# Optimization experiments

Measured on AMD Instinct MI355X. Metric: run time of the kernel, lower is better.

The kernel has to match this reference:

```python
import jax, jax.numpy as jnp
import numpy as np

N_NODES = 50000
N_EDGES = 600000
D_IN = 128
D_HID = 128
N_IDX = 4096


def gcn_conv(x, W, b, edge_index, num_nodes):
    """PyG GCNConv: add self loops, symmetric deg normalization, scatter-add, bias."""
    h = x @ W  # [N, D_out]
    loop = jnp.arange(num_nodes, dtype=edge_index.dtype)
    src = jnp.concatenate([edge_index[0], loop])
    dst = jnp.concatenate([edge_index[1], loop])
    deg = jax.ops.segment_sum(jnp.ones_like(dst, dtype=h.dtype), dst, num_segments=num_nodes)
    dinv = jnp.where(deg > 0, jax.lax.rsqrt(jnp.maximum(deg, 1.0)), 0.0)
    norm = dinv[src] * dinv[dst]  # [E+N]
    msgs = h[src] * norm[:, None]
    out = jax.ops.segment_sum(msgs, dst, num_segments=num_nodes)
    return out + b


def setup_inputs() -> dict:
    key = jax.random.key(0)
    ks = jax.random.split(key, 18)
    d = {
        "x": jax.random.normal(ks[0], (N_NODES, D_IN), dtype=jnp.float32),
        "syntactic_edge_index": jax.random.randint(ks[1], (2, N_EDGES), 0, N_NODES, dtype=jnp.int32),
        "sequential_edge_index": jax.random.randint(ks[2], (2, N_EDGES), 0, N_NODES, dtype=jnp.int32),
        "semantic_edge_index": jax.random.randint(ks[3], (2, N_EDGES), 0, N_NODES, dtype=jnp.int32),
        "index": jax.random.randint(ks[4], (N_IDX,), 0, N_NODES, dtype=jnp.int32),
    }
    s = 1.0 / np.sqrt(D_IN)
    names = ["syn", "seq", "sem"]
    for i, n in enumerate(names):
        d[f"w1_{n}"] = jax.random.uniform(ks[5 + i], (D_IN, D_HID), jnp.float32, -s, s)
        d[f"b1_{n}"] = jnp.zeros((D_HID,), jnp.float32)
        d[f"w2_{n}"] = jax.random.uniform(ks[8 + i], (D_HID, D_HID), jnp.float32, -s, s)
        d[f"b2_{n}"] = jnp.zeros((D_HID,), jnp.float32)
    return d


def reference(x, syntactic_edge_index, sequential_edge_index, semantic_edge_index, index,
              w1_syn, b1_syn, w1_seq, b1_seq, w1_sem, b1_sem,
              w2_syn, b2_syn, w2_seq, b2_seq, w2_sem, b2_sem):
    n = x.shape[0]
    # layer 1: three parallel GCN branches + ReLU (dropout is identity in eval mode)
    a = jax.nn.relu(gcn_conv(x, w1_syn, b1_syn, syntactic_edge_index, n))
    b = jax.nn.relu(gcn_conv(x, w1_seq, b1_seq, sequential_edge_index, n))
    c = jax.nn.relu(gcn_conv(x, w1_sem, b1_sem, semantic_edge_index, n))
    h = jnp.maximum(jnp.maximum(a, b), c)
    # layer 2
    a2 = jax.nn.relu(gcn_conv(h, w2_syn, b2_syn, syntactic_edge_index, n))
    b2 = jax.nn.relu(gcn_conv(h, w2_seq, b2_seq, sequential_edge_index, n))
    c2 = jax.nn.relu(gcn_conv(h, w2_sem, b2_sem, semantic_edge_index, n))
    out = jnp.maximum(jnp.maximum(a2, b2), c2)
    return out[index]
```

## Files before the change

kernel.cpp:

```cpp
#include <hip/hip_runtime.h>
#include <hip/hip_fp16.h>

#define NN 50000
#define NE 600000
#define NG 3
#define D  128
#define NI 4096
#define BW 1024
#define NBUCK 49
#define EPT_BIN 16
#define EPB_BIN (256 * EPT_BIN)
#define NBLK_BIN ((NE + EPB_BIN - 1) / EPB_BIN)
#define XCVT_BLKS 3125
#define WCVT_BLKS 48
#define CNT_BLKS (NBLK_BIN * NG)

typedef _Float16 half8 __attribute__((ext_vector_type(8)));
typedef _Float16 half4v __attribute__((ext_vector_type(4)));
typedef float floatx4 __attribute__((ext_vector_type(4)));

static __device__ __forceinline__ float wextract(unsigned int v) {
  unsigned short u = (unsigned short)(v >> 16);
  _Float16 h;
  __builtin_memcpy(&h, &u, 2);
  return (float)h;
}

static __device__ __forceinline__ unsigned int packsw(int s, float w) {
  _Float16 h = (_Float16)w;
  unsigned short u;
  __builtin_memcpy(&u, &h, 2);
  return (unsigned int)s | ((unsigned int)u << 16);
}

static __device__ __forceinline__ int bucket_scan(const int* bcnt, int g, int lane) {
  int v = (lane < NBUCK) ? bcnt[g * NBUCK + lane] : 0;
  int incl = v;
#pragma unroll
  for (int off = 1; off < 64; off <<= 1) {
    int t = __shfl_up(incl, off, 64);
    if (lane >= off) incl += t;
  }
  return incl - v;
}


__global__ __launch_bounds__(256) void prep_kernel(
    const float* __restrict__ x, __half* __restrict__ xh,
    const float* __restrict__ W0, const float* __restrict__ W1, const float* __restrict__ W2,
    const float* __restrict__ W3, const float* __restrict__ W4, const float* __restrict__ W5,
    __half* __restrict__ Wf,
    const int* __restrict__ e0, const int* __restrict__ e1, const int* __restrict__ e2,
    int* __restrict__ bucketCnt) {
  __shared__ int cnt[NBUCK];
  int blk = blockIdx.x;
  int tid = threadIdx.x;
  if (blk < XCVT_BLKS) {
    int i = blk * 256 + tid;
    size_t base = (size_t)i * 8;
    float4 v0 = *(const float4*)&x[base];
    float4 v1 = *(const float4*)&x[base + 4];
    half8 h;
    h[0] = (_Float16)v0.x; h[1] = (_Float16)v0.y; h[2] = (_Float16)v0.z; h[3] = (_Float16)v0.w;
    h[4] = (_Float16)v1.x; h[5] = (_Float16)v1.y; h[6] = (_Float16)v1.z; h[7] = (_Float16)v1.w;
    *(half8*)&xh[base] = h;
  } else if (blk < XCVT_BLKS + WCVT_BLKS) {
    const float* Wm[6] = {W0, W1, W2, W3, W4, W5};
    int t = (blk - XCVT_BLKS) * 256 + tid;
    int mat = t >> 11;
    int fr = (t >> 6) & 31;
    int lane = t & 63;
    int tt = fr >> 2, ks = fr & 3;
    int n = tt * 16 + (lane & 15);
    int kb = ks * 32 + (lane >> 4) * 8;
    const float* W = Wm[mat];
#pragma unroll
    for (int j = 0; j < 8; j++)
      Wf[(size_t)t * 8 + j] = __float2half(W[(kb + j) * 128 + n]);
  } else {
    int cb = blk - XCVT_BLKS - WCVT_BLKS;
    int g = cb / NBLK_BIN, eb = cb % NBLK_BIN;
    const int* ei = (g == 0) ? e0 : ((g == 1) ? e1 : e2);
    if (tid < NBUCK) cnt[tid] = 0;
    __syncthreads();
    int base = eb * EPB_BIN;
#pragma unroll
    for (int i = 0; i < EPT_BIN; i++) {
      int e = base + tid + i * 256;
      if (e < NE) atomicAdd(&cnt[ei[NE + e] >> 10], 1);
    }
    __syncthreads();
    if (tid < NBUCK) atomicAdd(&bucketCnt[g * NBUCK + tid], cnt[tid]);
  }
}

__global__ __launch_bounds__(256) void bin_kernel(const int* __restrict__ e0,
    const int* __restrict__ e1, const int* __restrict__ e2,
    const int* __restrict__ bcnt, int* __restrict__ cur0,
    unsigned int* __restrict__ binned) {
  __shared__ int cnt[4][NBUCK];
  __shared__ int sbase[NBUCK];
  __shared__ int base[NBUCK];
  __shared__ int woff[4][NBUCK];
  int g = blockIdx.y;
  const int* ei = (g == 0) ? e0 : ((g == 1) ? e1 : e2);
  int tid = threadIdx.x;
  int wave = tid >> 6;
  if (tid < 64) {
    int ex = bucket_scan(bcnt, g, tid);
    if (tid < NBUCK) sbase[tid] = ex;
  }
  if (tid < NBUCK) { cnt[0][tid] = 0; cnt[1][tid] = 0; cnt[2][tid] = 0; cnt[3][tid] = 0; }
  __syncthreads();
  int estart = blockIdx.x * EPB_BIN;
  int src[EPT_BIN], dst[EPT_BIN], rk[EPT_BIN];
#pragma unroll
  for (int i = 0; i < EPT_BIN; i++) {
    int e = estart + tid + i * 256;
    if (e < NE) {
      src[i] = ei[e];
      dst[i] = ei[NE + e];
      rk[i] = atomicAdd(&cnt[wave][dst[i] >> 10], 1);
    } else {
      rk[i] = -1;
    }
  }
  __syncthreads();
  if (tid < NBUCK) {
    int c0 = cnt[0][tid], c1 = cnt[1][tid], c2 = cnt[2][tid], c3 = cnt[3][tid];
    int total = c0 + c1 + c2 + c3;
    int wb = (total > 0) ? atomicAdd(&cur0[g * NBUCK + tid], total) : 0;
    base[tid] = sbase[tid] + wb;
    woff[0][tid] = 0; woff[1][tid] = c0; woff[2][tid] = c0 + c1; woff[3][tid] = c0 + c1 + c2;
  }
  __syncthreads();
#pragma unroll
  for (int i = 0; i < EPT_BIN; i++) {
    if (rk[i] >= 0) {
      int b = dst[i] >> 10;
      binned[(size_t)g * NE + base[b] + woff[wave][b] + rk[i]] =
          (unsigned int)src[i] | ((unsigned int)dst[i] << 16);
    }
  }
}

__global__ __launch_bounds__(256) void csr_kernel(const unsigned int* __restrict__ binned,
    const int* __restrict__ bcnt, int* __restrict__ rp, float* __restrict__ dinv) {
  __shared__ int deg[BW];
  __shared__ int wsum[4];
  __shared__ int sbb;
  int g = blockIdx.y, b = blockIdx.x;
  int tid = threadIdx.x;
  int node0 = b * BW;
  if (tid < 64) {
    int ex = bucket_scan(bcnt, g, tid);
    if (tid == b) sbb = ex;
  }
  if (b == 0 && tid == 0) rp[g * (NN + 1) + NN] = NE;
  for (int i = tid; i < BW; i += 256) deg[i] = 0;
  __syncthreads();
  int bb = sbb;
  int total = bcnt[g * NBUCK + b];
  const unsigned int* bp = binned + (size_t)g * NE + bb;
  for (int e = tid; e < total; e += 256) {
    unsigned int p = bp[e];
    atomicAdd(&deg[(int)(p >> 16) - node0], 1);
  }
  __syncthreads();
  int d0 = deg[tid * 4], d1 = deg[tid * 4 + 1], d2 = deg[tid * 4 + 2], d3 = deg[tid * 4 + 3];
  int s = d0 + d1 + d2 + d3;
  int lane = tid & 63;
  int incl = s;
#pragma unroll
  for (int off = 1; off < 64; off <<= 1) {
    int n = __shfl_up(incl, off, 64);
    if (lane >= off) incl += n;
  }
  if (lane == 63) wsum[tid >> 6] = incl;
  __syncthreads();
  int wbase = 0;
#pragma unroll
  for (int w = 0; w < 4; w++)
    if (w < (tid >> 6)) wbase += wsum[w];
  int ex = wbase + incl - s;
  int exs[4] = {ex, ex + d0, ex + d0 + d1, ex + d0 + d1 + d2};
  int ds[4] = {d0, d1, d2, d3};
#pragma unroll
  for (int k = 0; k < 4; k++) {
    int node = node0 + tid * 4 + k;
    if (node < NN) {
      rp[g * (NN + 1) + node] = bb + exs[k];
      dinv[g * NN + node] = rsqrtf((float)ds[k] + 1.0f);
    }
  }
}

__global__ __launch_bounds__(256) void fillp_kernel(const unsigned int* __restrict__ binned,
    const int* __restrict__ bcnt, const int* __restrict__ rp,
    const float* __restrict__ dinv, unsigned int* __restrict__ colp) {
  __shared__ int cur[BW];
  __shared__ int sbb;
  int g = blockIdx.y, b = blockIdx.x;
  int tid = threadIdx.x;
  int node0 = b * BW;
  if (tid < 64) {
    int ex = bucket_scan(bcnt, g, tid);
    if (tid == b) sbb = ex;
  }
  for (int i = tid; i < BW; i += 256) {
    int node = node0 + i;
    cur[i] = (node < NN) ? rp[g * (NN + 1) + node] : 0;
  }
  __syncthreads();
  int bb = sbb;
  int total = bcnt[g * NBUCK + b];
  const unsigned int* bp = binned + (size_t)g * NE + bb;
  for (int e = tid; e < total; e += 256) {
    unsigned int p = bp[e];
    int srcid = (int)(p & 0xffffu);
    int r = atomicAdd(&cur[(int)(p >> 16) - node0], 1);
    colp[(size_t)g * NE + r] = packsw(srcid, dinv[g * NN + srcid]);
  }
}


__global__ __launch_bounds__(256) void aggb_kernel(
    const __half* __restrict__ srch, const int* __restrict__ rp,
    const unsigned int* __restrict__ colp, const float* __restrict__ dinv,
    const int* __restrict__ index, __half* __restrict__ tout, int nrows) {
  int b = blockIdx.y;
  int w = (blockIdx.x * 256 + threadIdx.x) >> 6;
  if (w >= nrows) return;
  int lane = threadIdx.x & 63;
  int sub = lane >> 5;
  int fl = lane & 31;
  int node = index ? index[w] : w;
  const _Float16* srcv = (const _Float16*)srch;
  half4v selfh = *(const half4v*)&srcv[(size_t)node * D + fl * 4];
  float di = dinv[b * NN + node];
  float a[4];
#pragma unroll
  for (int k = 0; k < 4; k++) a[k] = sub ? 0.f : di * (float)selfh[k];
  const int* rpb = rp + b * (NN + 1);
  int s = rpb[node], e = rpb[node + 1];
  int n = e - s;
  const unsigned int* cp = colp + (size_t)b * NE;
  unsigned int c = (lane < n) ? cp[s + lane] : 0u;
  int m = min(n, 64);
  for (int j = 0; j < m; j += 16) {
    unsigned int v[8];
    float wg[8];
    half4v h[8];
#pragma unroll
    for (int u = 0; u < 8; u++) {
      v[u] = (unsigned int)__shfl((int)c, j + u * 2 + sub, 64);
      wg[u] = wextract(v[u]);
      h[u] = *(const half4v*)&srcv[(size_t)(v[u] & 0xffffu) * D + fl * 4];
    }
#pragma unroll
    for (int u = 0; u < 8; u++)
#pragma unroll
      for (int k = 0; k < 4; k++) a[k] = fmaf((float)h[u][k], wg[u], a[k]);
  }
  for (int q = s + 64; q < e; q += 64) {
    int nn = min(e - q, 64);
    unsigned int cc = (lane < nn) ? cp[q + lane] : 0u;
    for (int j = 0; j < nn; j += 2) {
      unsigned int v = (unsigned int)__shfl((int)cc, j + sub, 64);
      float wf = wextract(v);
      half4v hv = *(const half4v*)&srcv[(size_t)(v & 0xffffu) * D + fl * 4];
#pragma unroll
      for (int k = 0; k < 4; k++) a[k] = fmaf((float)hv[k], wf, a[k]);
    }
  }
#pragma unroll
  for (int k = 0; k < 4; k++) a[k] += __shfl_xor(a[k], 32, 64);
  if (sub == 0) {
    half4v o;
#pragma unroll
    for (int k = 0; k < 4; k++) o[k] = (_Float16)(di * a[k]);
    _Float16* tv = (_Float16*)tout;
    *(half4v*)&tv[(size_t)b * nrows * D + (size_t)w * D + fl * 4] = o;
  }
}


#define ALD 136

__global__ __launch_bounds__(256) void mmf_kernel(const __half* __restrict__ A,
    const __half* __restrict__ Wf,
    const float* __restrict__ B0, const float* __restrict__ B1, const float* __restrict__ B2,
    __half* __restrict__ outh, float* __restrict__ outf, int M) {
  __shared__ _Float16 As[128 * ALD];
  __shared__ _Float16 Ws[16384];
  const float* Bb[3] = {B0, B1, B2};
  const int tid = threadIdx.x;
  const int wave = tid >> 6, lane = tid & 63;
  const int wr = (wave >> 1) * 64, wc = (wave & 1) * 64;
  const int ln = lane & 15, quad = lane >> 4;
  const int row0 = blockIdx.x * 128;
  float om[4][4][4];

  for (int b = 0; b < 3; b++) {
    const __half* Wb = Wf + (size_t)b * 16384;
#pragma unroll
    for (int i = 0; i < 8; i++) {
      int id = tid + i * 256;
      *(half8*)&Ws[id * 8] = *(const half8*)&Wb[(size_t)id * 8];
    }
    const __half* Ab = A + (size_t)b * M * D;
#pragma unroll
    for (int i = 0; i < 8; i++) {
      int idx = tid + i * 256;
      int r = idx >> 4, c8 = idx & 15;
      int gr = row0 + r;
      gr = (gr < M) ? gr : (M - 1);
      half8 v = *(const half8*)&Ab[(size_t)gr * D + c8 * 8];
      *(half8*)&As[r * ALD + c8 * 8] = v;
    }
    __syncthreads();

    float bias[4];
#pragma unroll
    for (int ct = 0; ct < 4; ct++) bias[ct] = Bb[b][wc + ct * 16 + ln];
    floatx4 acc[4][4];
#pragma unroll
    for (int rt = 0; rt < 4; rt++)
#pragma unroll
      for (int ct = 0; ct < 4; ct++)
        acc[rt][ct] = (floatx4){bias[ct], bias[ct], bias[ct], bias[ct]};

#pragma unroll
    for (int ks = 0; ks < 4; ks++) {
      half8 av[4];
#pragma unroll
      for (int rt = 0; rt < 4; rt++)
        av[rt] = *(const half8*)&As[(wr + rt * 16 + ln) * ALD + ks * 32 + quad * 8];
#pragma unroll
      for (int ct = 0; ct < 4; ct++) {
        int tt = (wc >> 4) + ct;
        half8 bv = *(const half8*)&Ws[((tt * 4 + ks) * 64 + lane) * 8];
#pragma unroll
        for (int rt = 0; rt < 4; rt++)
          acc[rt][ct] = __builtin_amdgcn_mfma_f32_16x16x32_f16(av[rt], bv, acc[rt][ct], 0, 0, 0);
      }
    }
#pragma unroll
    for (int rt = 0; rt < 4; rt++)
#pragma unroll
      for (int ct = 0; ct < 4; ct++)
#pragma unroll
        for (int r = 0; r < 4; r++) {
          float v = fmaxf(acc[rt][ct][r], 0.f);
          om[rt][ct][r] = (b == 0) ? v : fmaxf(om[rt][ct][r], v);
        }
    __syncthreads();
  }
#pragma unroll
  for (int rt = 0; rt < 4; rt++) {
    int m = row0 + wr + rt * 16 + quad * 4;
#pragma unroll
    for (int r = 0; r < 4; r++) {
      if (m + r < M) {
#pragma unroll
        for (int ct = 0; ct < 4; ct++) {
          int n = wc + ct * 16 + ln;
          if (outh) outh[(size_t)(m + r) * D + n] = __float2half(om[rt][ct][r]);
          else      outf[(size_t)(m + r) * D + n] = om[rt][ct][r];
        }
      }
    }
  }
}


extern "C" void kernel_launch(void* const* d_in, const int* in_sizes, int n_in,
                              void* d_out, int out_size, void* d_ws, size_t ws_size,
                              hipStream_t stream) {
  const float* x = (const float*)d_in[0];
  const int* e0 = (const int*)d_in[1];
  const int* e1 = (const int*)d_in[2];
  const int* e2 = (const int*)d_in[3];
  const int* index = (const int*)d_in[4];
  const float* w1[3] = {(const float*)d_in[5], (const float*)d_in[9],  (const float*)d_in[13]};
  const float* b1[3] = {(const float*)d_in[6], (const float*)d_in[10], (const float*)d_in[14]};
  const float* w2[3] = {(const float*)d_in[7], (const float*)d_in[11], (const float*)d_in[15]};
  const float* b2[3] = {(const float*)d_in[8], (const float*)d_in[12], (const float*)d_in[16]};
  float* out = (float*)d_out;

  char* ws = (char*)d_ws;
  size_t o = 0;
  auto alloc = [&](size_t bytes) {
    o = (o + 255) & ~(size_t)255;
    void* p = ws + o;
    o += bytes;
    return p;
  };
  int*    rp     = (int*)alloc((size_t)NG * (NN + 1) * 4);
  unsigned int* colp = (unsigned int*)alloc((size_t)NG * NE * 4);
  float*  dinv   = (float*)alloc((size_t)NG * NN * 4);
  int*    bcnt   = (int*)alloc((size_t)2 * NG * NBUCK * 4);
  int*    cur0   = bcnt + NG * NBUCK;
  __half* xh     = (__half*)alloc((size_t)NN * D * 2);
  __half* Wf     = (__half*)alloc((size_t)6 * 128 * 128 * 2);
  __half* t1     = (__half*)alloc((size_t)NG * NN * D * 2);
  __half* hacc   = (__half*)alloc((size_t)NN * D * 2);
  unsigned int* binned = (unsigned int*)t1;
  __half* t2     = t1;
  (void)ws_size; (void)in_sizes; (void)n_in; (void)out_size;

  hipMemsetAsync(bcnt, 0, (size_t)2 * NG * NBUCK * 4, stream);
  prep_kernel<<<XCVT_BLKS + WCVT_BLKS + CNT_BLKS, 256, 0, stream>>>(
      x, xh, w1[0], w1[1], w1[2], w2[0], w2[1], w2[2], Wf, e0, e1, e2, bcnt);
  bin_kernel<<<dim3(NBLK_BIN, NG), 256, 0, stream>>>(e0, e1, e2, bcnt, cur0, binned);
  csr_kernel<<<dim3(NBUCK, NG), 256, 0, stream>>>(binned, bcnt, rp, dinv);
  fillp_kernel<<<dim3(NBUCK, NG), 256, 0, stream>>>(binned, bcnt, rp, dinv, colp);

  aggb_kernel<<<dim3((NN * 64 + 255) / 256, NG), 256, 0, stream>>>(
      xh, rp, colp, dinv, nullptr, t1, NN);
  mmf_kernel<<<(NN + 127) / 128, 256, 0, stream>>>(t1, Wf, b1[0], b1[1], b1[2],
                                                   hacc, nullptr, NN);
  aggb_kernel<<<dim3((NI * 64 + 255) / 256, NG), 256, 0, stream>>>(
      hacc, rp, colp, dinv, index, t2, NI);
  mmf_kernel<<<(NI + 127) / 128, 256, 0, stream>>>(t2, Wf + (size_t)3 * 16384,
                                                   b2[0], b2[1], b2[2], nullptr, out, NI);
}
```

Measured before the change: 279.1 us.

## Stage binned edges in LDS, shrink aggregation unroll, template GEMM row tile

The bin kernel now writes each block's edges into a shared-memory staging buffer ordered by bucket, then copies each bucket out contiguously. This aims to replace scattered global writes with coalesced ones. The aggregation kernel's first-chunk gather loop drops from 8 to 4 unrolled neighbours, cutting register pressure at the cost of fewer loads in flight. The GEMM kernel is templated on row tiles, and the small second-layer GEMM (4096 rows) uses 64-row blocks so more blocks are launched.

```diff
diff --git a/kernel.cpp b/kernel.cpp
--- a/kernel.cpp
+++ b/kernel.cpp
@@ -100,8 +100,11 @@
     unsigned int* __restrict__ binned) {
   __shared__ int cnt[4][NBUCK];
   __shared__ int sbase[NBUCK];
-  __shared__ int base[NBUCK];
+  __shared__ int gbase[NBUCK];
   __shared__ int woff[4][NBUCK];
+  __shared__ int tot[NBUCK];
+  __shared__ int lbase[NBUCK];
+  __shared__ unsigned int stage[EPB_BIN];
   int g = blockIdx.y;
   const int* ei = (g == 0) ? e0 : ((g == 1) ? e1 : e2);
   int tid = threadIdx.x;
@@ -129,18 +132,39 @@
   if (tid < NBUCK) {
     int c0 = cnt[0][tid], c1 = cnt[1][tid], c2 = cnt[2][tid], c3 = cnt[3][tid];
     int total = c0 + c1 + c2 + c3;
+    tot[tid] = total;
     int wb = (total > 0) ? atomicAdd(&cur0[g * NBUCK + tid], total) : 0;
-    base[tid] = sbase[tid] + wb;
+    gbase[tid] = sbase[tid] + wb;
     woff[0][tid] = 0; woff[1][tid] = c0; woff[2][tid] = c0 + c1; woff[3][tid] = c0 + c1 + c2;
+  }
+  __syncthreads();
+  if (tid < 64) {
+    int v = (tid < NBUCK) ? tot[tid] : 0;
+    int incl = v;
+#pragma unroll
+    for (int off = 1; off < 64; off <<= 1) {
+      int t = __shfl_up(incl, off, 64);
+      if (tid >= off) incl += t;
+    }
+    if (tid < NBUCK) lbase[tid] = incl - v;
   }
   __syncthreads();
 #pragma unroll
   for (int i = 0; i < EPT_BIN; i++) {
     if (rk[i] >= 0) {
       int b = dst[i] >> 10;
-      binned[(size_t)g * NE + base[b] + woff[wave][b] + rk[i]] =
+      stage[lbase[b] + woff[wave][b] + rk[i]] =
           (unsigned int)src[i] | ((unsigned int)dst[i] << 16);
     }
+  }
+  __syncthreads();
+  int ln = tid & 63;
+  for (int b = wave; b < NBUCK; b += 4) {
+    int len = tot[b];
+    int gb = gbase[b];
+    int lb = lbase[b];
+    for (int j = ln; j < len; j += 64)
+      binned[(size_t)g * NE + gb + j] = stage[lb + j];
   }
 }
 
@@ -247,18 +271,17 @@
   const unsigned int* cp = colp + (size_t)b * NE;
   unsigned int c = (lane < n) ? cp[s + lane] : 0u;
   int m = min(n, 64);
-  for (int j = 0; j < m; j += 16) {
-    unsigned int v[8];
-    float wg[8];
-    half4v h[8];
-#pragma unroll
-    for (int u = 0; u < 8; u++) {
-      v[u] = (unsigned int)__shfl((int)c, j + u * 2 + sub, 64);
-      wg[u] = wextract(v[u]);
-      h[u] = *(const half4v*)&srcv[(size_t)(v[u] & 0xffffu) * D + fl * 4];
-    }
-#pragma unroll
-    for (int u = 0; u < 8; u++)
+  for (int j = 0; j < m; j += 8) {
+    half4v h[4];
+    float wg[4];
+#pragma unroll
+    for (int u = 0; u < 4; u++) {
+      unsigned int v = (unsigned int)__shfl((int)c, j + u * 2 + sub, 64);
+      wg[u] = wextract(v);
+      h[u] = *(const half4v*)&srcv[(size_t)(v & 0xffffu) * D + fl * 4];
+    }
+#pragma unroll
+    for (int u = 0; u < 4; u++)
 #pragma unroll
       for (int k = 0; k < 4; k++) a[k] = fmaf((float)h[u][k], wg[u], a[k]);
   }
@@ -287,19 +310,20 @@
 
 #define ALD 136
 
+template <int RT>
 __global__ __launch_bounds__(256) void mmf_kernel(const __half* __restrict__ A,
     const __half* __restrict__ Wf,
     const float* __restrict__ B0, const float* __restrict__ B1, const float* __restrict__ B2,
     __half* __restrict__ outh, float* __restrict__ outf, int M) {
-  __shared__ _Float16 As[128 * ALD];
+  __shared__ _Float16 As[RT * 32 * ALD];
   __shared__ _Float16 Ws[16384];
   const float* Bb[3] = {B0, B1, B2};
   const int tid = threadIdx.x;
   const int wave = tid >> 6, lane = tid & 63;
-  const int wr = (wave >> 1) * 64, wc = (wave & 1) * 64;
+  const int wr = (wave >> 1) * (RT * 16), wc = (wave & 1) * 64;
   const int ln = lane & 15, quad = lane >> 4;
-  const int row0 = blockIdx.x * 128;
-  float om[4][4][4];
+  const int row0 = blockIdx.x * (RT * 32);
+  float om[RT][4][4];
 
   for (int b = 0; b < 3; b++) {
     const __half* Wb = Wf + (size_t)b * 16384;
@@ -310,7 +334,7 @@
     }
     const __half* Ab = A + (size_t)b * M * D;
 #pragma unroll
-    for (int i = 0; i < 8; i++) {
+    for (int i = 0; i < RT * 2; i++) {
       int idx = tid + i * 256;
       int r = idx >> 4, c8 = idx & 15;
       int gr = row0 + r;
@@ -323,30 +347,30 @@
     float bias[4];
 #pragma unroll
     for (int ct = 0; ct < 4; ct++) bias[ct] = Bb[b][wc + ct * 16 + ln];
-    floatx4 acc[4][4];
-#pragma unroll
-    for (int rt = 0; rt < 4; rt++)
+    floatx4 acc[RT][4];
+#pragma unroll
+    for (int rt = 0; rt < RT; rt++)
 #pragma unroll
       for (int ct = 0; ct < 4; ct++)
         acc[rt][ct] = (floatx4){bias[ct], bias[ct], bias[ct], bias[ct]};
 
 #pragma unroll
     for (int ks = 0; ks < 4; ks++) {
-      half8 av[4];
-#pragma unroll
-      for (int rt = 0; rt < 4; rt++)
+      half8 av[RT];
+#pragma unroll
+      for (int rt = 0; rt < RT; rt++)
         av[rt] = *(const half8*)&As[(wr + rt * 16 + ln) * ALD + ks * 32 + quad * 8];
 #pragma unroll
       for (int ct = 0; ct < 4; ct++) {
         int tt = (wc >> 4) + ct;
         half8 bv = *(const half8*)&Ws[((tt * 4 + ks) * 64 + lane) * 8];
 #pragma unroll
-        for (int rt = 0; rt < 4; rt++)
+        for (int rt = 0; rt < RT; rt++)
           acc[rt][ct] = __builtin_amdgcn_mfma_f32_16x16x32_f16(av[rt], bv, acc[rt][ct], 0, 0, 0);
       }
     }
 #pragma unroll
-    for (int rt = 0; rt < 4; rt++)
+    for (int rt = 0; rt < RT; rt++)
 #pragma unroll
       for (int ct = 0; ct < 4; ct++)
 #pragma unroll
@@ -357,7 +381,7 @@
     __syncthreads();
   }
 #pragma unroll
-  for (int rt = 0; rt < 4; rt++) {
+  for (int rt = 0; rt < RT; rt++) {
     int m = row0 + wr + rt * 16 + quad * 4;
 #pragma unroll
     for (int r = 0; r < 4; r++) {
@@ -418,10 +442,10 @@
 
   aggb_kernel<<<dim3((NN * 64 + 255) / 256, NG), 256, 0, stream>>>(
       xh, rp, colp, dinv, nullptr, t1, NN);
-  mmf_kernel<<<(NN + 127) / 128, 256, 0, stream>>>(t1, Wf, b1[0], b1[1], b1[2],
-                                                   hacc, nullptr, NN);
+  mmf_kernel<4><<<(NN + 127) / 128, 256, 0, stream>>>(t1, Wf, b1[0], b1[1], b1[2],
+                                                      hacc, nullptr, NN);
   aggb_kernel<<<dim3((NI * 64 + 255) / 256, NG), 256, 0, stream>>>(
       hacc, rp, colp, dinv, index, t2, NI);
-  mmf_kernel<<<(NI + 127) / 128, 256, 0, stream>>>(t2, Wf + (size_t)3 * 16384,
-                                                   b2[0], b2[1], b2[2], nullptr, out, NI);
-}
+  mmf_kernel<2><<<(NI + 63) / 64, 256, 0, stream>>>(t2, Wf + (size_t)3 * 16384,
+                                                    b2[0], b2[1], b2[2], nullptr, out, NI);
+}
```

Result: no change. 282.0 us (+1.0%).
